# Kernel tuning notes

Measured on AMD Instinct MI355X. Metric: run time of the kernel, lower is better.

The kernel has to match this reference:

```python
import jax, jax.numpy as jnp
import numpy as np

B, T = 1024, 8192


def setup_inputs() -> dict:
    key = jax.random.key(0)
    k1, k2 = jax.random.split(key)
    # phi/psi are [B, T, 2] probability-bound robustness traces in [0, 1]
    phi = jax.random.uniform(k1, (B, T, 2), dtype=jnp.float32)
    psi = jax.random.uniform(k2, (B, T, 2), dtype=jnp.float32)
    return {"phi": phi, "psi": psi}


def reference(phi, psi):
    """Until operator, interval [0, inf), exact (scale<=0) min/max.

    Original O(T^2) double loop computes, for each t:
        out[t] = max_{tau in [t, T-1]} min( min(phi[t..tau-1]), psi[tau] )
    with the empty segment (tau == t) contributing min(ones, psi[t]).
    Because min distributes over max, this satisfies the exact O(T)
    backward recurrence:
        r[t] = max( min(1, psi[t]), min(phi[t], r[t+1]) ),  r[T] = -inf
    which we evaluate with a reversed lax.scan over the time axis.
    """
    phi_t = jnp.swapaxes(phi, 0, 1)  # [T, B, 2]
    psi_t = jnp.swapaxes(psi, 0, 1)  # [T, B, 2]

    def step(carry, xs):
        p, q = xs
        v = jnp.minimum(jnp.asarray(1.0, p.dtype), q)  # tau == t term (min with ones)
        r = jnp.maximum(v, jnp.minimum(p, carry))
        return r, r

    init = jnp.full(phi_t.shape[1:], -jnp.inf, dtype=phi.dtype)  # [B, 2]
    _, out = jax.lax.scan(step, init, (phi_t, psi_t), reverse=True)
    return jnp.swapaxes(out, 0, 1)  # [B, T, 2]
```

## Files before the change

### kernel.cpp

```cpp
#include <hip/hip_runtime.h>


#define T_LEN 8192
#define NSEG  8
#define BLOCK (NSEG * 64)

__device__ __forceinline__ float rfl(float x) {
    return __int_as_float(__builtin_amdgcn_readfirstlane(__float_as_int(x)));
}

__device__ __forceinline__ void wave_lds_fence() {
    __asm__ volatile("" ::: "memory");
    __builtin_amdgcn_wave_barrier();
    __asm__ volatile("" ::: "memory");
}

__global__ __launch_bounds__(BLOCK, 8) void until_kernel(
    const float* __restrict__ phi, const float* __restrict__ psi,
    float* __restrict__ out)
{
    const int  row  = blockIdx.x;
    const int  tid  = threadIdx.x;
    const int  w    = tid >> 6;
    const int  lane = tid & 63;
    const float NEG = -__builtin_huge_valf();
    const float POS =  __builtin_huge_valf();

    const size_t segf4 = (size_t)row * (T_LEN / 2) + (size_t)w * 512;
    const float4* __restrict__ phi4 = (const float4*)phi + segf4;
    const float4* __restrict__ psi4 = (const float4*)psi + segf4;
    float4* __restrict__ out4 = (float4*)out + segf4;

    __shared__ alignas(16) float lds[NSEG * 1024];
    __shared__ float4 ssum[NSEG];
    float* wl = lds + w * 1024;

    float4 GAx[2], GAy[2], GBx[2], GBy[2];
    float  Sax[2], Say[2], Sbx[2], Sby[2];

#pragma unroll
    for (int r = 0; r < 2; ++r) {
        if (r) wave_lds_fence();

        float4 P[4], Q[4];
#pragma unroll
        for (int kl = 0; kl < 4; ++kl) {
            P[kl] = phi4[(r * 4 + kl) * 64 + lane];
            Q[kl] = psi4[(r * 4 + kl) * 64 + lane];
        }

#pragma unroll
        for (int kl = 0; kl < 4; ++kl) {
            float* base = wl + kl * 64 + lane;
            float v0x = fminf(1.f, Q[kl].x), v0y = fminf(1.f, Q[kl].y);
            float v1x = fminf(1.f, Q[kl].z), v1y = fminf(1.f, Q[kl].w);
            base[0]   = fmaxf(v0x, fminf(P[kl].x, v1x));
            base[256] = fmaxf(v0y, fminf(P[kl].y, v1y));
            base[512] = fminf(P[kl].x, P[kl].z);
            base[768] = fminf(P[kl].y, P[kl].w);
        }
        wave_lds_fence();

        GAx[r] = *(const float4*)(wl + 0 * 256 + lane * 4);
        GAy[r] = *(const float4*)(wl + 1 * 256 + lane * 4);
        GBx[r] = *(const float4*)(wl + 2 * 256 + lane * 4);
        GBy[r] = *(const float4*)(wl + 3 * 256 + lane * 4);

        float hax = GAx[r].w, hay = GAy[r].w, hbx = GBx[r].w, hby = GBy[r].w;
        hax = fmaxf(GAx[r].z, fminf(GBx[r].z, hax));
        hay = fmaxf(GAy[r].z, fminf(GBy[r].z, hay));
        hbx = fminf(GBx[r].z, hbx);
        hby = fminf(GBy[r].z, hby);
        hax = fmaxf(GAx[r].y, fminf(GBx[r].y, hax));
        hay = fmaxf(GAy[r].y, fminf(GBy[r].y, hay));
        hbx = fminf(GBx[r].y, hbx);
        hby = fminf(GBy[r].y, hby);
        hax = fmaxf(GAx[r].x, fminf(GBx[r].x, hax));
        hay = fmaxf(GAy[r].x, fminf(GBy[r].x, hay));
        hbx = fminf(GBx[r].x, hbx);
        hby = fminf(GBy[r].x, hby);

#pragma unroll
        for (int off = 1; off < 64; off <<= 1) {
            float gax = __shfl_down(hax, off), gay = __shfl_down(hay, off);
            float gbx = __shfl_down(hbx, off), gby = __shfl_down(hby, off);
            bool  val = (lane + off) < 64;
            gax = val ? gax : NEG;  gay = val ? gay : NEG;
            gbx = val ? gbx : POS;  gby = val ? gby : POS;
            hax = fmaxf(hax, fminf(hbx, gax));
            hay = fmaxf(hay, fminf(hby, gay));
            hbx = fminf(hbx, gbx);
            hby = fminf(hby, gby);
        }
        Sax[r] = hax; Say[r] = hay; Sbx[r] = hbx; Sby[r] = hby;
    }

    float R0ax = rfl(Sax[0]), R0ay = rfl(Say[0]);
    float R0bx = rfl(Sbx[0]), R0by = rfl(Sby[0]);
    float R1ax = rfl(Sax[1]), R1ay = rfl(Say[1]);
    float R1bx = rfl(Sbx[1]), R1by = rfl(Sby[1]);
    if (lane == 0) {
        float wax = fmaxf(R0ax, fminf(R0bx, R1ax));
        float way = fmaxf(R0ay, fminf(R0by, R1ay));
        float wbx = fminf(R0bx, R1bx);
        float wby = fminf(R0by, R1by);
        ssum[w] = make_float4(wax, way, wbx, wby);
    }
    __syncthreads();
    float rcx = NEG, rcy = NEG;
    for (int j = NSEG - 1; j > w; --j) {
        float4 s = ssum[j];
        rcx = fmaxf(s.x, fminf(s.z, rcx));
        rcy = fmaxf(s.y, fminf(s.w, rcy));
    }

    float rinx[2], riny[2];
    rinx[1] = rcx;
    riny[1] = rcy;
    rinx[0] = fmaxf(R1ax, fminf(R1bx, rcx));
    riny[0] = fmaxf(R1ay, fminf(R1by, rcy));

    wave_lds_fence();
#pragma unroll
    for (int r = 0; r < 2; ++r) {
        float yx = fmaxf(Sax[r], fminf(Sbx[r], rinx[r]));
        float yy = fmaxf(Say[r], fminf(Sby[r], riny[r]));
        float cx = __shfl_down(yx, 1), cy = __shfl_down(yy, 1);
        if (lane == 63) { cx = rinx[r]; cy = riny[r]; }
        float4 CX, CY;
        CX.w = cx;
        CY.w = cy;
        CX.z = fmaxf(GAx[r].w, fminf(GBx[r].w, CX.w));
        CY.z = fmaxf(GAy[r].w, fminf(GBy[r].w, CY.w));
        CX.y = fmaxf(GAx[r].z, fminf(GBx[r].z, CX.z));
        CY.y = fmaxf(GAy[r].z, fminf(GBy[r].z, CY.z));
        CX.x = fmaxf(GAx[r].y, fminf(GBx[r].y, CX.y));
        CY.x = fmaxf(GAy[r].y, fminf(GBy[r].y, CY.y));
        *(float4*)(wl +       r * 256 + lane * 4) = CX;
        *(float4*)(wl + 512 + r * 256 + lane * 4) = CY;
    }
    wave_lds_fence();

#pragma unroll
    for (int k = 0; k < 8; ++k) {
        const int e = k * 64 + lane;
        float4 P2 = phi4[e];
        float4 Q2 = psi4[e];
        float cx = wl[e];
        float cy = wl[512 + e];
        float r1x = fmaxf(fminf(1.f, Q2.z), fminf(P2.z, cx));
        float r1y = fmaxf(fminf(1.f, Q2.w), fminf(P2.w, cy));
        float r0x = fmaxf(fminf(1.f, Q2.x), fminf(P2.x, r1x));
        float r0y = fmaxf(fminf(1.f, Q2.y), fminf(P2.y, r1y));
        out4[e] = make_float4(r0x, r0y, r1x, r1y);
    }
}

extern "C" void kernel_launch(void* const* d_in, const int* in_sizes, int n_in,
                              void* d_out, int out_size, void* d_ws, size_t ws_size,
                              hipStream_t stream) {
    const float* phi = (const float*)d_in[0];
    const float* psi = (const float*)d_in[1];
    float* out = (float*)d_out;
    const int Bn = in_sizes[0] / (T_LEN * 2);
    until_kernel<<<Bn, BLOCK, 0, stream>>>(phi, psi, out);
}
```

Before: 195.2 us.

## Process two rows per block with software-prefetched loads across chunks

Each block now handles two batch rows and keeps the next chunk's phi/psi loads in flight while the current chunk is written to LDS and scanned. This hides global load latency behind the per-chunk scan work. The full __syncthreads is replaced by a raw s_barrier with an lgkmcnt wait, and launch bounds drop to 4 blocks per CU. The cost is half as many blocks, more registers per thread and a second block-wide barrier per block; the grid also assumes the batch size is even.

```diff
diff --git a/kernel.cpp b/kernel.cpp
--- a/kernel.cpp
+++ b/kernel.cpp
@@ -4,6 +4,7 @@
 #define T_LEN 8192
 #define NSEG  8
 #define BLOCK (NSEG * 64)
+#define RPB   2
 
 __device__ __forceinline__ float rfl(float x) {
     return __int_as_float(__builtin_amdgcn_readfirstlane(__float_as_int(x)));
@@ -15,144 +16,168 @@
     __asm__ volatile("" ::: "memory");
 }
 
-__global__ __launch_bounds__(BLOCK, 8) void until_kernel(
-    const float* __restrict__ phi, const float* __restrict__ psi,
-    float* __restrict__ out)
+__device__ __forceinline__ void block_lds_barrier() {
+    __asm__ volatile("s_waitcnt lgkmcnt(0)" ::: "memory");
+    __builtin_amdgcn_s_barrier();
+    __asm__ volatile("" ::: "memory");
+}
+
+__global__ __launch_bounds__(BLOCK, 4) void until_kernel(
+    const float* __restrict__ phi_, const float* __restrict__ psi_,
+    float* __restrict__ out_)
 {
-    const int  row  = blockIdx.x;
+    const int  bid  = blockIdx.x;
     const int  tid  = threadIdx.x;
     const int  w    = tid >> 6;
     const int  lane = tid & 63;
     const float NEG = -__builtin_huge_valf();
     const float POS =  __builtin_huge_valf();
 
-    const size_t segf4 = (size_t)row * (T_LEN / 2) + (size_t)w * 512;
-    const float4* __restrict__ phi4 = (const float4*)phi + segf4;
-    const float4* __restrict__ psi4 = (const float4*)psi + segf4;
-    float4* __restrict__ out4 = (float4*)out + segf4;
+    const float4* __restrict__ phi4 = (const float4*)phi_;
+    const float4* __restrict__ psi4 = (const float4*)psi_;
+    float4* __restrict__ out4 = (float4*)out_;
+
+    const size_t rb[RPB] = {
+        (size_t)(RPB * bid + 0) * (T_LEN / 2) + (size_t)w * 512,
+        (size_t)(RPB * bid + 1) * (T_LEN / 2) + (size_t)w * 512
+    };
 
     __shared__ alignas(16) float lds[NSEG * 1024];
-    __shared__ float4 ssum[NSEG];
+    __shared__ float4 ssum[RPB][NSEG];
     float* wl = lds + w * 1024;
 
-    float4 GAx[2], GAy[2], GBx[2], GBy[2];
-    float  Sax[2], Say[2], Sbx[2], Sby[2];
+    float4 P[4], Q[4];
+#pragma unroll
+    for (int kl = 0; kl < 4; ++kl) {
+        P[kl] = phi4[rb[0] + kl * 64 + lane];
+        Q[kl] = psi4[rb[0] + kl * 64 + lane];
+    }
 
 #pragma unroll
-    for (int r = 0; r < 2; ++r) {
-        if (r) wave_lds_fence();
+    for (int row = 0; row < RPB; ++row) {
+        float4 GAx[2], GAy[2], GBx[2], GBy[2];
+        float  Sax[2], Say[2], Sbx[2], Sby[2];
 
-        float4 P[4], Q[4];
 #pragma unroll
-        for (int kl = 0; kl < 4; ++kl) {
-            P[kl] = phi4[(r * 4 + kl) * 64 + lane];
-            Q[kl] = psi4[(r * 4 + kl) * 64 + lane];
+        for (int r = 0; r < 2; ++r) {
+            if (row + r) wave_lds_fence();
+
+#pragma unroll
+            for (int kl = 0; kl < 4; ++kl) {
+                float* base = wl + kl * 64 + lane;
+                float v0x = fminf(1.f, Q[kl].x), v0y = fminf(1.f, Q[kl].y);
+                float v1x = fminf(1.f, Q[kl].z), v1y = fminf(1.f, Q[kl].w);
+                base[0]   = fmaxf(v0x, fminf(P[kl].x, v1x));
+                base[256] = fmaxf(v0y, fminf(P[kl].y, v1y));
+                base[512] = fminf(P[kl].x, P[kl].z);
+                base[768] = fminf(P[kl].y, P[kl].w);
+            }
+
+            const int s = row * 2 + r;
+            if (s < RPB * 2 - 1) {
+                const size_t nb  = rb[(s + 1) >> 1];
+                const int    nrd = (s + 1) & 1;
+#pragma unroll
+                for (int kl = 0; kl < 4; ++kl) {
+                    P[kl] = phi4[nb + (nrd * 4 + kl) * 64 + lane];
+                    Q[kl] = psi4[nb + (nrd * 4 + kl) * 64 + lane];
+                }
+            }
+            wave_lds_fence();
+
+            GAx[r] = *(const float4*)(wl + 0 * 256 + lane * 4);
+            GAy[r] = *(const float4*)(wl + 1 * 256 + lane * 4);
+            GBx[r] = *(const float4*)(wl + 2 * 256 + lane * 4);
+            GBy[r] = *(const float4*)(wl + 3 * 256 + lane * 4);
+
+            float hax = GAx[r].w, hay = GAy[r].w, hbx = GBx[r].w, hby = GBy[r].w;
+            hax = fmaxf(GAx[r].z, fminf(GBx[r].z, hax));
+            hay = fmaxf(GAy[r].z, fminf(GBy[r].z, hay));
+            hbx = fminf(GBx[r].z, hbx);
+            hby = fminf(GBy[r].z, hby);
+            hax = fmaxf(GAx[r].y, fminf(GBx[r].y, hax));
+            hay = fmaxf(GAy[r].y, fminf(GBy[r].y, hay));
+            hbx = fminf(GBx[r].y, hbx);
+            hby = fminf(GBy[r].y, hby);
+            hax = fmaxf(GAx[r].x, fminf(GBx[r].x, hax));
+            hay = fmaxf(GAy[r].x, fminf(GBy[r].x, hay));
+            hbx = fminf(GBx[r].x, hbx);
+            hby = fminf(GBy[r].x, hby);
+
+#pragma unroll
+            for (int off = 1; off < 64; off <<= 1) {
+                float gax = __shfl_down(hax, off), gay = __shfl_down(hay, off);
+                float gbx = __shfl_down(hbx, off), gby = __shfl_down(hby, off);
+                bool  val = (lane + off) < 64;
+                gax = val ? gax : NEG;  gay = val ? gay : NEG;
+                gbx = val ? gbx : POS;  gby = val ? gby : POS;
+                hax = fmaxf(hax, fminf(hbx, gax));
+                hay = fmaxf(hay, fminf(hby, gay));
+                hbx = fminf(hbx, gbx);
+                hby = fminf(hby, gby);
+            }
+            Sax[r] = hax; Say[r] = hay; Sbx[r] = hbx; Sby[r] = hby;
         }
 
+        float R0ax = rfl(Sax[0]), R0ay = rfl(Say[0]);
+        float R0bx = rfl(Sbx[0]), R0by = rfl(Sby[0]);
+        float R1ax = rfl(Sax[1]), R1ay = rfl(Say[1]);
+        float R1bx = rfl(Sbx[1]), R1by = rfl(Sby[1]);
+        if (lane == 0) {
+            float wax = fmaxf(R0ax, fminf(R0bx, R1ax));
+            float way = fmaxf(R0ay, fminf(R0by, R1ay));
+            float wbx = fminf(R0bx, R1bx);
+            float wby = fminf(R0by, R1by);
+            ssum[row][w] = make_float4(wax, way, wbx, wby);
+        }
+        block_lds_barrier();
+        float rcx = NEG, rcy = NEG;
+        for (int j = NSEG - 1; j > w; --j) {
+            float4 s4 = ssum[row][j];
+            rcx = fmaxf(s4.x, fminf(s4.z, rcx));
+            rcy = fmaxf(s4.y, fminf(s4.w, rcy));
+        }
+
+        float rinx[2], riny[2];
+        rinx[1] = rcx;
+        riny[1] = rcy;
+        rinx[0] = fmaxf(R1ax, fminf(R1bx, rcx));
+        riny[0] = fmaxf(R1ay, fminf(R1by, rcy));
+
+        wave_lds_fence();
 #pragma unroll
-        for (int kl = 0; kl < 4; ++kl) {
-            float* base = wl + kl * 64 + lane;
-            float v0x = fminf(1.f, Q[kl].x), v0y = fminf(1.f, Q[kl].y);
-            float v1x = fminf(1.f, Q[kl].z), v1y = fminf(1.f, Q[kl].w);
-            base[0]   = fmaxf(v0x, fminf(P[kl].x, v1x));
-            base[256] = fmaxf(v0y, fminf(P[kl].y, v1y));
-            base[512] = fminf(P[kl].x, P[kl].z);
-            base[768] = fminf(P[kl].y, P[kl].w);
+        for (int r = 0; r < 2; ++r) {
+            float yx = fmaxf(Sax[r], fminf(Sbx[r], rinx[r]));
+            float yy = fmaxf(Say[r], fminf(Sby[r], riny[r]));
+            float cx = __shfl_down(yx, 1), cy = __shfl_down(yy, 1);
+            if (lane == 63) { cx = rinx[r]; cy = riny[r]; }
+            float4 CX, CY;
+            CX.w = cx;
+            CY.w = cy;
+            CX.z = fmaxf(GAx[r].w, fminf(GBx[r].w, CX.w));
+            CY.z = fmaxf(GAy[r].w, fminf(GBy[r].w, CY.w));
+            CX.y = fmaxf(GAx[r].z, fminf(GBx[r].z, CX.z));
+            CY.y = fmaxf(GAy[r].z, fminf(GBy[r].z, CY.z));
+            CX.x = fmaxf(GAx[r].y, fminf(GBx[r].y, CX.y));
+            CY.x = fmaxf(GAy[r].y, fminf(GBy[r].y, CY.y));
+            *(float4*)(wl +       r * 256 + lane * 4) = CX;
+            *(float4*)(wl + 512 + r * 256 + lane * 4) = CY;
         }
         wave_lds_fence();
 
-        GAx[r] = *(const float4*)(wl + 0 * 256 + lane * 4);
-        GAy[r] = *(const float4*)(wl + 1 * 256 + lane * 4);
-        GBx[r] = *(const float4*)(wl + 2 * 256 + lane * 4);
-        GBy[r] = *(const float4*)(wl + 3 * 256 + lane * 4);
-
-        float hax = GAx[r].w, hay = GAy[r].w, hbx = GBx[r].w, hby = GBy[r].w;
-        hax = fmaxf(GAx[r].z, fminf(GBx[r].z, hax));
-        hay = fmaxf(GAy[r].z, fminf(GBy[r].z, hay));
-        hbx = fminf(GBx[r].z, hbx);
-        hby = fminf(GBy[r].z, hby);
-        hax = fmaxf(GAx[r].y, fminf(GBx[r].y, hax));
-        hay = fmaxf(GAy[r].y, fminf(GBy[r].y, hay));
-        hbx = fminf(GBx[r].y, hbx);
-        hby = fminf(GBy[r].y, hby);
-        hax = fmaxf(GAx[r].x, fminf(GBx[r].x, hax));
-        hay = fmaxf(GAy[r].x, fminf(GBy[r].x, hay));
-        hbx = fminf(GBx[r].x, hbx);
-        hby = fminf(GBy[r].x, hby);
-
 #pragma unroll
-        for (int off = 1; off < 64; off <<= 1) {
-            float gax = __shfl_down(hax, off), gay = __shfl_down(hay, off);
-            float gbx = __shfl_down(hbx, off), gby = __shfl_down(hby, off);
-            bool  val = (lane + off) < 64;
-            gax = val ? gax : NEG;  gay = val ? gay : NEG;
-            gbx = val ? gbx : POS;  gby = val ? gby : POS;
-            hax = fmaxf(hax, fminf(hbx, gax));
-            hay = fmaxf(hay, fminf(hby, gay));
-            hbx = fminf(hbx, gbx);
-            hby = fminf(hby, gby);
+        for (int k = 0; k < 8; ++k) {
+            const int e = k * 64 + lane;
+            float4 P2 = phi4[rb[row] + e];
+            float4 Q2 = psi4[rb[row] + e];
+            float cx = wl[e];
+            float cy = wl[512 + e];
+            float r1x = fmaxf(fminf(1.f, Q2.z), fminf(P2.z, cx));
+            float r1y = fmaxf(fminf(1.f, Q2.w), fminf(P2.w, cy));
+            float r0x = fmaxf(fminf(1.f, Q2.x), fminf(P2.x, r1x));
+            float r0y = fmaxf(fminf(1.f, Q2.y), fminf(P2.y, r1y));
+            out4[rb[row] + e] = make_float4(r0x, r0y, r1x, r1y);
         }
-        Sax[r] = hax; Say[r] = hay; Sbx[r] = hbx; Sby[r] = hby;
-    }
-
-    float R0ax = rfl(Sax[0]), R0ay = rfl(Say[0]);
-    float R0bx = rfl(Sbx[0]), R0by = rfl(Sby[0]);
-    float R1ax = rfl(Sax[1]), R1ay = rfl(Say[1]);
-    float R1bx = rfl(Sbx[1]), R1by = rfl(Sby[1]);
-    if (lane == 0) {
-        float wax = fmaxf(R0ax, fminf(R0bx, R1ax));
-        float way = fmaxf(R0ay, fminf(R0by, R1ay));
-        float wbx = fminf(R0bx, R1bx);
-        float wby = fminf(R0by, R1by);
-        ssum[w] = make_float4(wax, way, wbx, wby);
-    }
-    __syncthreads();
-    float rcx = NEG, rcy = NEG;
-    for (int j = NSEG - 1; j > w; --j) {
-        float4 s = ssum[j];
-        rcx = fmaxf(s.x, fminf(s.z, rcx));
-        rcy = fmaxf(s.y, fminf(s.w, rcy));
-    }
-
-    float rinx[2], riny[2];
-    rinx[1] = rcx;
-    riny[1] = rcy;
-    rinx[0] = fmaxf(R1ax, fminf(R1bx, rcx));
-    riny[0] = fmaxf(R1ay, fminf(R1by, rcy));
-
-    wave_lds_fence();
-#pragma unroll
-    for (int r = 0; r < 2; ++r) {
-        float yx = fmaxf(Sax[r], fminf(Sbx[r], rinx[r]));
-        float yy = fmaxf(Say[r], fminf(Sby[r], riny[r]));
-        float cx = __shfl_down(yx, 1), cy = __shfl_down(yy, 1);
-        if (lane == 63) { cx = rinx[r]; cy = riny[r]; }
-        float4 CX, CY;
-        CX.w = cx;
-        CY.w = cy;
-        CX.z = fmaxf(GAx[r].w, fminf(GBx[r].w, CX.w));
-        CY.z = fmaxf(GAy[r].w, fminf(GBy[r].w, CY.w));
-        CX.y = fmaxf(GAx[r].z, fminf(GBx[r].z, CX.z));
-        CY.y = fmaxf(GAy[r].z, fminf(GBy[r].z, CY.z));
-        CX.x = fmaxf(GAx[r].y, fminf(GBx[r].y, CX.y));
-        CY.x = fmaxf(GAy[r].y, fminf(GBy[r].y, CY.y));
-        *(float4*)(wl +       r * 256 + lane * 4) = CX;
-        *(float4*)(wl + 512 + r * 256 + lane * 4) = CY;
-    }
-    wave_lds_fence();
-
-#pragma unroll
-    for (int k = 0; k < 8; ++k) {
-        const int e = k * 64 + lane;
-        float4 P2 = phi4[e];
-        float4 Q2 = psi4[e];
-        float cx = wl[e];
-        float cy = wl[512 + e];
-        float r1x = fmaxf(fminf(1.f, Q2.z), fminf(P2.z, cx));
-        float r1y = fmaxf(fminf(1.f, Q2.w), fminf(P2.w, cy));
-        float r0x = fmaxf(fminf(1.f, Q2.x), fminf(P2.x, r1x));
-        float r0y = fmaxf(fminf(1.f, Q2.y), fminf(P2.y, r1y));
-        out4[e] = make_float4(r0x, r0y, r1x, r1y);
     }
 }
 
@@ -163,5 +188,5 @@
     const float* psi = (const float*)d_in[1];
     float* out = (float*)d_out;
     const int Bn = in_sizes[0] / (T_LEN * 2);
-    until_kernel<<<Bn, BLOCK, 0, stream>>>(phi, psi, out);
+    until_kernel<<<Bn / RPB, BLOCK, 0, stream>>>(phi, psi, out);
 }
```

Result: faster. 181.7 us (-6.9%).
